# Kernel optimization log

Measured on AMD Instinct MI355X. Metric: run time of the kernel, lower is better.

Reference implementation:

```python
import jax, jax.numpy as jnp
import numpy as np

B, N, DIN, DOUT = 32, 1024, 256, 256


def setup_inputs() -> dict:
    key = jax.random.key(0)
    ks = jax.random.split(key, 7)
    s = 1.0 / np.sqrt(DIN)
    return {
        "x": jax.random.normal(ks[0], (B, N, DIN), dtype=jnp.float32),
        "Wq": jax.random.uniform(ks[1], (DOUT, DIN), minval=-s, maxval=s, dtype=jnp.float32),
        "bq": jax.random.uniform(ks[2], (DOUT,), minval=-s, maxval=s, dtype=jnp.float32),
        "Wk": jax.random.uniform(ks[3], (DOUT, DIN), minval=-s, maxval=s, dtype=jnp.float32),
        "bk": jax.random.uniform(ks[4], (DOUT,), minval=-s, maxval=s, dtype=jnp.float32),
        "Wv": jax.random.uniform(ks[5], (DOUT, DIN), minval=-s, maxval=s, dtype=jnp.float32),
        "bv": jax.random.uniform(ks[6], (DOUT,), minval=-s, maxval=s, dtype=jnp.float32),
    }


def reference(x, Wq, bq, Wk, bk, Wv, bv):
    # q, k, v: (B, N, Dout)
    q = jnp.einsum("bnd,od->bno", x, Wq) + bq
    k = jnp.einsum("bnd,od->bno", x, Wk) + bk
    v = jnp.einsum("bnd,od->bno", x, Wv) + bv
    # logits: (B, N, N) = q @ k^T per batch
    logits = jnp.einsum("bnd,bmd->bnm", q, k)
    # NOTE: softmax over the BATCH dim (axis=0), as in the original module
    attn = jax.nn.softmax(logits, axis=0)
    out = jnp.einsum("bnm,bmd->bnd", attn, v)  # (B, N, Dout)
    return out
```

## Files before the change

kernel.cpp:

```cpp
#include <hip/hip_runtime.h>

typedef __bf16 bf16x8 __attribute__((ext_vector_type(8)));
typedef __bf16 bf16x4 __attribute__((ext_vector_type(4)));
typedef float  f32x4  __attribute__((ext_vector_type(4)));

__device__ __forceinline__ void g2l16(const void* g, void* l) {
    __builtin_amdgcn_global_load_lds((const __attribute__((address_space(1))) void*)g,
                                     (__attribute__((address_space(3))) void*)l, 16, 0, 0);
}

template<int MCH, int NCH>
__device__ __forceinline__ void gemm_core(
    const __bf16* __restrict__ At, const __bf16* __restrict__ Bt,
    int lda, int ldb, int K,
    __bf16* As, __bf16* Bs, f32x4 (&acc)[MCH][NCH], int tid)
{
    const int w = tid >> 6, lane = tid & 63;
    const int quad = lane >> 4, l16 = lane & 15;
    const int wm = w & 1, wn = w >> 1;

    const int srow = (w << 3) + (lane >> 3);
    const int scol = ((lane & 7) ^ (lane >> 3)) << 3;
    char* ldsA = (char*)As + (size_t)w * 1024;
    char* ldsB = (char*)Bs + (size_t)w * 1024;
    const __bf16* Ag = At + (size_t)srow * lda + scol;
    const __bf16* Bg = Bt + (size_t)srow * ldb + scol;

    for (int k0 = 0; k0 < K; k0 += 64) {
        __syncthreads();
        #pragma unroll
        for (int c = 0; c < MCH; c++)
            g2l16(Ag + (size_t)(c * 32) * lda + k0, ldsA + c * 4096);
        #pragma unroll
        for (int c = 0; c < NCH; c++)
            g2l16(Bg + (size_t)(c * 32) * ldb + k0, ldsB + c * 4096);
        __syncthreads();

        #pragma unroll
        for (int kk = 0; kk < 64; kk += 32) {
            const int ub = kk >> 3;
            bf16x8 a[MCH], b[NCH];
            #pragma unroll
            for (int mt = 0; mt < MCH; mt++) {
                const int row = wm * (MCH * 16) + mt * 16 + l16;
                a[mt] = *(const bf16x8*)&As[row * 64 + (((quad + ub) ^ (row & 7)) << 3)];
            }
            #pragma unroll
            for (int nt = 0; nt < NCH; nt++) {
                const int row = wn * (NCH * 16) + nt * 16 + l16;
                b[nt] = *(const bf16x8*)&Bs[row * 64 + (((quad + ub) ^ (row & 7)) << 3)];
            }
            #pragma unroll
            for (int mt = 0; mt < MCH; mt++)
                #pragma unroll
                for (int nt = 0; nt < NCH; nt++)
                    acc[mt][nt] = __builtin_amdgcn_mfma_f32_16x16x32_bf16(
                        a[mt], b[nt], acc[mt][nt], 0, 0, 0);
        }
    }
}


__global__ __launch_bounds__(256)
void gemm_proj(const __bf16* __restrict__ xb, const __bf16* __restrict__ Wb,
               const float* __restrict__ bpack, __bf16* __restrict__ qkv,
               __bf16* __restrict__ vT)
{
    __shared__ __align__(16) __bf16 As[128 * 64];
    __shared__ __align__(16) __bf16 Bs[128 * 64];
    const int tid = threadIdx.x;
    const int id  = blockIdx.x;
    const int z   = id >> 9;
    const int rr  = id & 511;

    const __bf16 *At, *Bt;
    int m0, n0;
    if (z < 2) {
        m0 = (rr & 1) * 128; n0 = (rr >> 1) * 128;
        At = Wb + z * 131072 + m0 * 256;
        Bt = xb + (size_t)n0 * 256;
    } else {
        m0 = (rr >> 1) * 128; n0 = (rr & 1) * 128;
        At = xb + (size_t)m0 * 256;
        Bt = Wb + 2 * 131072 + n0 * 256;
    }

    f32x4 acc[4][4] = {};
    gemm_core<4, 4>(At, Bt, 256, 256, 256, As, Bs, acc, tid);

    const int w = tid >> 6, lane = tid & 63, quad = lane >> 4, l16 = lane & 15;
    const int wm = w & 1, wn = w >> 1;
    #pragma unroll
    for (int mt = 0; mt < 4; mt++) {
        const int i0 = m0 + wm * 64 + mt * 16 + quad * 4;
        #pragma unroll
        for (int nt = 0; nt < 4; nt++) {
            const int j = n0 + wn * 64 + nt * 16 + l16;
            bf16x4 pk;
            if (z < 2) {
                const f32x4 bn = *(const f32x4*)&bpack[z * 256 + i0];
                #pragma unroll
                for (int r = 0; r < 4; r++) pk[r] = (__bf16)(acc[mt][nt][r] + bn[r]);
                *(bf16x4*)(qkv + (size_t)z * 8388608 + (size_t)j * 256 + i0) = pk;
            } else {
                const float bn = bpack[512 + j];
                #pragma unroll
                for (int r = 0; r < 4; r++) pk[r] = (__bf16)(acc[mt][nt][r] + bn);
                *(bf16x4*)(vT + (size_t)j * 32768 + i0) = pk;
            }
        }
    }
}

__global__ __launch_bounds__(256)
void gemm_logits(const __bf16* __restrict__ qb, const __bf16* __restrict__ kb,
                 __bf16* __restrict__ E)
{
    __shared__ __align__(16) __bf16 As[128 * 64];
    __shared__ __align__(16) __bf16 Bs[128 * 64];
    const int tid = threadIdx.x;
    const int id  = blockIdx.x;
    const int x = id & 7, s = id >> 3;
    const int z = x + ((s >> 6) << 3);
    const int t = s & 63;
    const int m0 = (t & 7) * 128;
    const int n0 = (t >> 3) * 128;

    const __bf16* At = kb + (size_t)z * 262144 + m0 * 256;
    const __bf16* Bt = qb + (size_t)z * 262144 + n0 * 256;

    f32x4 acc[4][4] = {};
    gemm_core<4, 4>(At, Bt, 256, 256, 256, As, Bs, acc, tid);

    const int w = tid >> 6, lane = tid & 63, quad = lane >> 4, l16 = lane & 15;
    const int wm = w & 1, wn = w >> 1;
    __bf16* Eb = E + (size_t)z * 1048576;
    #pragma unroll
    for (int mt = 0; mt < 4; mt++) {
        const int i0 = m0 + wm * 64 + mt * 16 + quad * 4;
        #pragma unroll
        for (int nt = 0; nt < 4; nt++) {
            const int j = n0 + wn * 64 + nt * 16 + l16;
            bf16x4 pk;
            #pragma unroll
            for (int r = 0; r < 4; r++) pk[r] = (__bf16)__expf(acc[mt][nt][r]);
            *(bf16x4*)(Eb + (size_t)j * 1024 + i0) = pk;
        }
    }
}

__global__ __launch_bounds__(256)
void gemm_pv(const __bf16* __restrict__ vT, const __bf16* __restrict__ E,
             float* __restrict__ out)
{
    __shared__ __align__(16) __bf16 As[64 * 64];
    __shared__ __align__(16) __bf16 Bs[128 * 64];
    const int tid = threadIdx.x;
    const int id  = blockIdx.x;
    const int x = id & 7, s = id >> 3;
    const int z = x + ((s >> 5) << 3);
    const int t = s & 31;
    const int m0 = (t & 3) * 64;
    const int n0 = (t >> 2) * 128;

    const __bf16* At = vT + (size_t)m0 * 32768 + z * 1024;
    const __bf16* Bt = E + (size_t)z * 1048576 + (size_t)n0 * 1024;

    f32x4 acc[2][4] = {};
    gemm_core<2, 4>(At, Bt, 32768, 1024, 1024, As, Bs, acc, tid);

    const int w = tid >> 6, lane = tid & 63, quad = lane >> 4, l16 = lane & 15;
    const int wm = w & 1, wn = w >> 1;
    float* Ob = out + (size_t)z * 262144;
    #pragma unroll
    for (int mt = 0; mt < 2; mt++) {
        const int i0 = m0 + wm * 32 + mt * 16 + quad * 4;
        #pragma unroll
        for (int nt = 0; nt < 4; nt++) {
            const int j = n0 + wn * 64 + nt * 16 + l16;
            *(f32x4*)(Ob + (size_t)j * 256 + i0) = acc[mt][nt];
        }
    }
}

__global__ __launch_bounds__(256)
void cvt_all(const float* __restrict__ x,
             const float* __restrict__ Wq, const float* __restrict__ Wk,
             const float* __restrict__ Wv,
             const float* __restrict__ bq, const float* __restrict__ bk,
             const float* __restrict__ bv,
             __bf16* __restrict__ xb, __bf16* __restrict__ Wqb,
             float* __restrict__ bpack)
{
    const int i = blockIdx.x * 256 + threadIdx.x;
    if (i < 1073152) {
        const float* s; __bf16* d; int off;
        if (i < 1048576)      { s = x;  d = xb;            off = i; }
        else if (i < 1056768) { s = Wq; d = Wqb;           off = i - 1048576; }
        else if (i < 1064960) { s = Wk; d = Wqb + 131072;  off = i - 1056768; }
        else                  { s = Wv; d = Wqb + 262144;  off = i - 1064960; }
        const float4* s4 = (const float4*)s;
        const float4 f0 = s4[off * 2], f1 = s4[off * 2 + 1];
        bf16x8 o;
        o[0] = (__bf16)f0.x; o[1] = (__bf16)f0.y; o[2] = (__bf16)f0.z; o[3] = (__bf16)f0.w;
        o[4] = (__bf16)f1.x; o[5] = (__bf16)f1.y; o[6] = (__bf16)f1.z; o[7] = (__bf16)f1.w;
        ((bf16x8*)d)[off] = o;
    } else if (i < 1073344) {
        const int j = i - 1073152;
        const int sel = j >> 6, jj = j & 63;
        const float* s = sel == 0 ? bq : (sel == 1 ? bk : bv);
        ((float4*)bpack)[j] = ((const float4*)s)[jj];
    }
}

__global__ __launch_bounds__(256)
void softmax_norm(__bf16* __restrict__ E)
{
    const size_t p = (size_t)blockIdx.x * 256 + threadIdx.x;
    bf16x8* E8 = (bf16x8*)E;
    bf16x8 e[32];
    #pragma unroll
    for (int b = 0; b < 32; b++) e[b] = E8[(size_t)b * 131072 + p];
    float s[8] = {0.f, 0.f, 0.f, 0.f, 0.f, 0.f, 0.f, 0.f};
    #pragma unroll
    for (int b = 0; b < 32; b++)
        #pragma unroll
        for (int j = 0; j < 8; j++) s[j] += (float)e[b][j];
    float rs[8];
    #pragma unroll
    for (int j = 0; j < 8; j++) rs[j] = __builtin_amdgcn_rcpf(s[j]);
    #pragma unroll
    for (int b = 0; b < 32; b++) {
        bf16x8 o = e[b];
        #pragma unroll
        for (int j = 0; j < 8; j++) o[j] = (__bf16)((float)o[j] * rs[j]);
        E8[(size_t)b * 131072 + p] = o;
    }
}

extern "C" void kernel_launch(void* const* d_in, const int* in_sizes, int n_in,
                              void* d_out, int out_size, void* d_ws, size_t ws_size,
                              hipStream_t stream)
{
    const float* x  = (const float*)d_in[0];
    const float* Wq = (const float*)d_in[1];
    const float* bq = (const float*)d_in[2];
    const float* Wk = (const float*)d_in[3];
    const float* bk = (const float*)d_in[4];
    const float* Wv = (const float*)d_in[5];
    const float* bv = (const float*)d_in[6];
    float* out = (float*)d_out;

    char* ws = (char*)d_ws;
    __bf16* xb    = (__bf16*)(ws);
    __bf16* qkv   = (__bf16*)(ws + (16u << 20));
    __bf16* vT    = (__bf16*)(ws + (48u << 20));
    __bf16* E     = (__bf16*)(ws + (64u << 20));
    __bf16* Wqb   = (__bf16*)(ws + (128u << 20));
    float*  bpack = (float*) (ws + (128u << 20) + (3u << 18));

    cvt_all<<<4194, 256, 0, stream>>>(x, Wq, Wk, Wv, bq, bk, bv, xb, Wqb, bpack);

    gemm_proj<<<1536, 256, 0, stream>>>(xb, Wqb, bpack, qkv, vT);

    gemm_logits<<<2048, 256, 0, stream>>>(qkv, qkv + 8388608, E);

    softmax_norm<<<512, 256, 0, stream>>>(E);

    gemm_pv<<<1024, 256, 0, stream>>>(vT, E, out);
}
```

Measured before the change: 203.8 us.

## Fuse all stages into one persistent kernel with grid-wide atomic barriers

Replaces the five separate launches (convert, projection, logits, softmax, PV) with a single persistent kernel of 512 blocks. The blocks loop over tiles of each stage and synchronise with a global atomic-counter barrier between stages. Tile shapes and output layouts also change: projection uses 128x64 tiles and writes q/k row-major, and PV now reads E as the A operand, which changes the E and vT layouts. This removes launch gaps and tail effects between stages. In exchange it risks barrier spin overhead, deadlock if all 512 blocks are not co-resident, and scalar bf16 stores in the epilogues that are less coalesced.

```diff
diff --git a/kernel.cpp b/kernel.cpp
--- a/kernel.cpp
+++ b/kernel.cpp
@@ -61,181 +61,193 @@
 }
 
 
-__global__ __launch_bounds__(256)
-void gemm_proj(const __bf16* __restrict__ xb, const __bf16* __restrict__ Wb,
-               const float* __restrict__ bpack, __bf16* __restrict__ qkv,
-               __bf16* __restrict__ vT)
+__device__ __forceinline__ void cvt_piece(
+    int i, const float* x, const float* Wq, const float* Wk, const float* Wv,
+    __bf16* xb, __bf16* Wqb)
+{
+    const float* s; __bf16* d; int off;
+    if (i < 1048576)      { s = x;  d = xb;            off = i; }
+    else if (i < 1056768) { s = Wq; d = Wqb;           off = i - 1048576; }
+    else if (i < 1064960) { s = Wk; d = Wqb + 131072;  off = i - 1056768; }
+    else                  { s = Wv; d = Wqb + 262144;  off = i - 1064960; }
+    const float4 f0 = ((const float4*)s)[off * 2];
+    const float4 f1 = ((const float4*)s)[off * 2 + 1];
+    bf16x8 o;
+    o[0] = (__bf16)f0.x; o[1] = (__bf16)f0.y; o[2] = (__bf16)f0.z; o[3] = (__bf16)f0.w;
+    o[4] = (__bf16)f1.x; o[5] = (__bf16)f1.y; o[6] = (__bf16)f1.z; o[7] = (__bf16)f1.w;
+    ((bf16x8*)d)[off] = o;
+}
+
+__device__ __forceinline__ void proj_tile(
+    int t, const __bf16* xb, const __bf16* Wqb, const float* bpack,
+    __bf16* qkv, __bf16* vT, __bf16* As, __bf16* Bs, int tid)
+{
+    const int z = t >> 10, lc = t & 1023;
+    const int m0 = (lc & 255) * 128;
+    const int n0 = (lc >> 8) * 64;
+    f32x4 acc[4][2] = {};
+    gemm_core<4, 2>(xb + (size_t)m0 * 256, Wqb + z * 131072 + n0 * 256,
+                    256, 256, 256, As, Bs, acc, tid);
+    const int w = tid >> 6, lane = tid & 63, quad = lane >> 4, l16 = lane & 15;
+    const int wm = w & 1, wn = w >> 1;
+    #pragma unroll
+    for (int mt = 0; mt < 4; mt++) {
+        const int mb = m0 + wm * 64 + mt * 16 + quad * 4;
+        #pragma unroll
+        for (int nt = 0; nt < 2; nt++) {
+            const int n = n0 + wn * 32 + nt * 16 + l16;
+            if (z < 2) {
+                const float bn = bpack[z * 256 + n];
+                __bf16* C = qkv + (size_t)z * 8388608;
+                #pragma unroll
+                for (int r = 0; r < 4; r++)
+                    C[(size_t)(mb + r) * 256 + n] = (__bf16)(acc[mt][nt][r] + bn);
+            } else {
+                const float bn = bpack[512 + n];
+                bf16x4 pk;
+                #pragma unroll
+                for (int r = 0; r < 4; r++) pk[r] = (__bf16)(acc[mt][nt][r] + bn);
+                *(bf16x4*)(vT + (size_t)(mb >> 10) * 262144
+                           + (size_t)n * 1024 + (mb & 1023)) = pk;
+            }
+        }
+    }
+}
+
+__device__ __forceinline__ void logits_tile(
+    int id, const __bf16* qkv, __bf16* E, __bf16* As, __bf16* Bs, int tid)
+{
+    const int x8 = id & 7, s = id >> 3;
+    const int z  = x8 + ((s >> 6) << 3);
+    const int t  = s & 63;
+    const int m0 = (t & 7) * 128;
+    const int n0 = (t >> 3) * 128;
+    f32x4 acc[4][4] = {};
+    gemm_core<4, 4>(qkv + (size_t)z * 262144 + m0 * 256,
+                    qkv + 8388608 + (size_t)z * 262144 + n0 * 256,
+                    256, 256, 256, As, Bs, acc, tid);
+    const int w = tid >> 6, lane = tid & 63, quad = lane >> 4, l16 = lane & 15;
+    const int wm = w & 1, wn = w >> 1;
+    __bf16* Eb = E + (size_t)z * 1048576;
+    #pragma unroll
+    for (int mt = 0; mt < 4; mt++) {
+        const int mb = m0 + wm * 64 + mt * 16 + quad * 4;
+        #pragma unroll
+        for (int nt = 0; nt < 4; nt++) {
+            const int n = n0 + wn * 64 + nt * 16 + l16;
+            #pragma unroll
+            for (int r = 0; r < 4; r++)
+                Eb[(size_t)(mb + r) * 1024 + n] = (__bf16)__expf(acc[mt][nt][r]);
+        }
+    }
+}
+
+__device__ __forceinline__ void softmax_unit(int p, __bf16* E)
+{
+    bf16x4* E4 = (bf16x4*)E;
+    bf16x4 e[32];
+    #pragma unroll
+    for (int b = 0; b < 32; b++) e[b] = E4[(size_t)b * 262144 + p];
+    float sm[4] = {0.f, 0.f, 0.f, 0.f};
+    #pragma unroll
+    for (int b = 0; b < 32; b++)
+        #pragma unroll
+        for (int j = 0; j < 4; j++) sm[j] += (float)e[b][j];
+    float rs[4];
+    #pragma unroll
+    for (int j = 0; j < 4; j++) rs[j] = __builtin_amdgcn_rcpf(sm[j]);
+    #pragma unroll
+    for (int b = 0; b < 32; b++) {
+        bf16x4 o;
+        #pragma unroll
+        for (int j = 0; j < 4; j++) o[j] = (__bf16)((float)e[b][j] * rs[j]);
+        E4[(size_t)b * 262144 + p] = o;
+    }
+}
+
+__device__ __forceinline__ void pv_tile(
+    int id, const __bf16* E, const __bf16* vT, float* out,
+    __bf16* As, __bf16* Bs, int tid)
+{
+    const int x8 = id & 7, s = id >> 3;
+    const int z  = x8 + ((s >> 5) << 3);
+    const int t  = s & 31;
+    const int m0 = (t & 7) * 128;
+    const int n0 = (t >> 3) * 64;
+    f32x4 acc[4][2] = {};
+    gemm_core<4, 2>(E + (size_t)z * 1048576 + (size_t)m0 * 1024,
+                    vT + (size_t)z * 262144 + (size_t)n0 * 1024,
+                    1024, 1024, 1024, As, Bs, acc, tid);
+    const int w = tid >> 6, lane = tid & 63, quad = lane >> 4, l16 = lane & 15;
+    const int wm = w & 1, wn = w >> 1;
+    float* Ob = out + (size_t)z * 262144;
+    #pragma unroll
+    for (int mt = 0; mt < 4; mt++) {
+        const int mb = m0 + wm * 64 + mt * 16 + quad * 4;
+        #pragma unroll
+        for (int nt = 0; nt < 2; nt++) {
+            const int n = n0 + wn * 32 + nt * 16 + l16;
+            #pragma unroll
+            for (int r = 0; r < 4; r++)
+                Ob[(size_t)(mb + r) * 256 + n] = acc[mt][nt][r];
+        }
+    }
+}
+
+__device__ __forceinline__ void gbar(unsigned int* ctr, unsigned int target)
+{
+    __syncthreads();
+    if (threadIdx.x == 0) {
+        __threadfence();
+        __hip_atomic_fetch_add(ctr, 1u, __ATOMIC_RELAXED, __HIP_MEMORY_SCOPE_AGENT);
+        while (__hip_atomic_load(ctr, __ATOMIC_RELAXED, __HIP_MEMORY_SCOPE_AGENT)
+               < target)
+            __builtin_amdgcn_s_sleep(8);
+        __threadfence();
+    }
+    __syncthreads();
+}
+
+__global__ __launch_bounds__(256, 2)
+void mega(const float* __restrict__ x,  const float* __restrict__ Wq,
+          const float* __restrict__ bq, const float* __restrict__ Wk,
+          const float* __restrict__ bk, const float* __restrict__ Wv,
+          const float* __restrict__ bv,
+          __bf16* __restrict__ xb,  __bf16* __restrict__ qkv,
+          __bf16* __restrict__ vT,  __bf16* __restrict__ E,
+          __bf16* __restrict__ Wqb, float* __restrict__ bpack,
+          unsigned int* __restrict__ bar, float* __restrict__ out)
 {
     __shared__ __align__(16) __bf16 As[128 * 64];
     __shared__ __align__(16) __bf16 Bs[128 * 64];
-    const int tid = threadIdx.x;
-    const int id  = blockIdx.x;
-    const int z   = id >> 9;
-    const int rr  = id & 511;
-
-    const __bf16 *At, *Bt;
-    int m0, n0;
-    if (z < 2) {
-        m0 = (rr & 1) * 128; n0 = (rr >> 1) * 128;
-        At = Wb + z * 131072 + m0 * 256;
-        Bt = xb + (size_t)n0 * 256;
-    } else {
-        m0 = (rr >> 1) * 128; n0 = (rr & 1) * 128;
-        At = xb + (size_t)m0 * 256;
-        Bt = Wb + 2 * 131072 + n0 * 256;
-    }
-
-    f32x4 acc[4][4] = {};
-    gemm_core<4, 4>(At, Bt, 256, 256, 256, As, Bs, acc, tid);
-
-    const int w = tid >> 6, lane = tid & 63, quad = lane >> 4, l16 = lane & 15;
-    const int wm = w & 1, wn = w >> 1;
-    #pragma unroll
-    for (int mt = 0; mt < 4; mt++) {
-        const int i0 = m0 + wm * 64 + mt * 16 + quad * 4;
-        #pragma unroll
-        for (int nt = 0; nt < 4; nt++) {
-            const int j = n0 + wn * 64 + nt * 16 + l16;
-            bf16x4 pk;
-            if (z < 2) {
-                const f32x4 bn = *(const f32x4*)&bpack[z * 256 + i0];
-                #pragma unroll
-                for (int r = 0; r < 4; r++) pk[r] = (__bf16)(acc[mt][nt][r] + bn[r]);
-                *(bf16x4*)(qkv + (size_t)z * 8388608 + (size_t)j * 256 + i0) = pk;
-            } else {
-                const float bn = bpack[512 + j];
-                #pragma unroll
-                for (int r = 0; r < 4; r++) pk[r] = (__bf16)(acc[mt][nt][r] + bn);
-                *(bf16x4*)(vT + (size_t)j * 32768 + i0) = pk;
-            }
-        }
-    }
-}
-
-__global__ __launch_bounds__(256)
-void gemm_logits(const __bf16* __restrict__ qb, const __bf16* __restrict__ kb,
-                 __bf16* __restrict__ E)
-{
-    __shared__ __align__(16) __bf16 As[128 * 64];
-    __shared__ __align__(16) __bf16 Bs[128 * 64];
-    const int tid = threadIdx.x;
-    const int id  = blockIdx.x;
-    const int x = id & 7, s = id >> 3;
-    const int z = x + ((s >> 6) << 3);
-    const int t = s & 63;
-    const int m0 = (t & 7) * 128;
-    const int n0 = (t >> 3) * 128;
-
-    const __bf16* At = kb + (size_t)z * 262144 + m0 * 256;
-    const __bf16* Bt = qb + (size_t)z * 262144 + n0 * 256;
-
-    f32x4 acc[4][4] = {};
-    gemm_core<4, 4>(At, Bt, 256, 256, 256, As, Bs, acc, tid);
-
-    const int w = tid >> 6, lane = tid & 63, quad = lane >> 4, l16 = lane & 15;
-    const int wm = w & 1, wn = w >> 1;
-    __bf16* Eb = E + (size_t)z * 1048576;
-    #pragma unroll
-    for (int mt = 0; mt < 4; mt++) {
-        const int i0 = m0 + wm * 64 + mt * 16 + quad * 4;
-        #pragma unroll
-        for (int nt = 0; nt < 4; nt++) {
-            const int j = n0 + wn * 64 + nt * 16 + l16;
-            bf16x4 pk;
-            #pragma unroll
-            for (int r = 0; r < 4; r++) pk[r] = (__bf16)__expf(acc[mt][nt][r]);
-            *(bf16x4*)(Eb + (size_t)j * 1024 + i0) = pk;
-        }
-    }
-}
-
-__global__ __launch_bounds__(256)
-void gemm_pv(const __bf16* __restrict__ vT, const __bf16* __restrict__ E,
-             float* __restrict__ out)
-{
-    __shared__ __align__(16) __bf16 As[64 * 64];
-    __shared__ __align__(16) __bf16 Bs[128 * 64];
-    const int tid = threadIdx.x;
-    const int id  = blockIdx.x;
-    const int x = id & 7, s = id >> 3;
-    const int z = x + ((s >> 5) << 3);
-    const int t = s & 31;
-    const int m0 = (t & 3) * 64;
-    const int n0 = (t >> 2) * 128;
-
-    const __bf16* At = vT + (size_t)m0 * 32768 + z * 1024;
-    const __bf16* Bt = E + (size_t)z * 1048576 + (size_t)n0 * 1024;
-
-    f32x4 acc[2][4] = {};
-    gemm_core<2, 4>(At, Bt, 32768, 1024, 1024, As, Bs, acc, tid);
-
-    const int w = tid >> 6, lane = tid & 63, quad = lane >> 4, l16 = lane & 15;
-    const int wm = w & 1, wn = w >> 1;
-    float* Ob = out + (size_t)z * 262144;
-    #pragma unroll
-    for (int mt = 0; mt < 2; mt++) {
-        const int i0 = m0 + wm * 32 + mt * 16 + quad * 4;
-        #pragma unroll
-        for (int nt = 0; nt < 4; nt++) {
-            const int j = n0 + wn * 64 + nt * 16 + l16;
-            *(f32x4*)(Ob + (size_t)j * 256 + i0) = acc[mt][nt];
-        }
-    }
-}
-
-__global__ __launch_bounds__(256)
-void cvt_all(const float* __restrict__ x,
-             const float* __restrict__ Wq, const float* __restrict__ Wk,
-             const float* __restrict__ Wv,
-             const float* __restrict__ bq, const float* __restrict__ bk,
-             const float* __restrict__ bv,
-             __bf16* __restrict__ xb, __bf16* __restrict__ Wqb,
-             float* __restrict__ bpack)
-{
-    const int i = blockIdx.x * 256 + threadIdx.x;
-    if (i < 1073152) {
-        const float* s; __bf16* d; int off;
-        if (i < 1048576)      { s = x;  d = xb;            off = i; }
-        else if (i < 1056768) { s = Wq; d = Wqb;           off = i - 1048576; }
-        else if (i < 1064960) { s = Wk; d = Wqb + 131072;  off = i - 1056768; }
-        else                  { s = Wv; d = Wqb + 262144;  off = i - 1064960; }
-        const float4* s4 = (const float4*)s;
-        const float4 f0 = s4[off * 2], f1 = s4[off * 2 + 1];
-        bf16x8 o;
-        o[0] = (__bf16)f0.x; o[1] = (__bf16)f0.y; o[2] = (__bf16)f0.z; o[3] = (__bf16)f0.w;
-        o[4] = (__bf16)f1.x; o[5] = (__bf16)f1.y; o[6] = (__bf16)f1.z; o[7] = (__bf16)f1.w;
-        ((bf16x8*)d)[off] = o;
-    } else if (i < 1073344) {
-        const int j = i - 1073152;
-        const int sel = j >> 6, jj = j & 63;
-        const float* s = sel == 0 ? bq : (sel == 1 ? bk : bv);
-        ((float4*)bpack)[j] = ((const float4*)s)[jj];
-    }
-}
-
-__global__ __launch_bounds__(256)
-void softmax_norm(__bf16* __restrict__ E)
-{
-    const size_t p = (size_t)blockIdx.x * 256 + threadIdx.x;
-    bf16x8* E8 = (bf16x8*)E;
-    bf16x8 e[32];
-    #pragma unroll
-    for (int b = 0; b < 32; b++) e[b] = E8[(size_t)b * 131072 + p];
-    float s[8] = {0.f, 0.f, 0.f, 0.f, 0.f, 0.f, 0.f, 0.f};
-    #pragma unroll
-    for (int b = 0; b < 32; b++)
-        #pragma unroll
-        for (int j = 0; j < 8; j++) s[j] += (float)e[b][j];
-    float rs[8];
-    #pragma unroll
-    for (int j = 0; j < 8; j++) rs[j] = __builtin_amdgcn_rcpf(s[j]);
-    #pragma unroll
-    for (int b = 0; b < 32; b++) {
-        bf16x8 o = e[b];
-        #pragma unroll
-        for (int j = 0; j < 8; j++) o[j] = (__bf16)((float)o[j] * rs[j]);
-        E8[(size_t)b * 131072 + p] = o;
-    }
+    const int tid = threadIdx.x, blk = blockIdx.x;
+
+    {
+        const int g0 = blk * 256 + tid;
+        for (int i = g0; i < 1073152; i += 131072)
+            cvt_piece(i, x, Wq, Wk, Wv, xb, Wqb);
+        if (g0 < 192) {
+            const int sel = g0 >> 6, jj = g0 & 63;
+            const float* s = sel == 0 ? bq : (sel == 1 ? bk : bv);
+            ((float4*)bpack)[g0] = ((const float4*)s)[jj];
+        }
+    }
+    gbar(bar, 512);
+
+    for (int it = 0; it < 6; it++)
+        proj_tile(blk + it * 512, xb, Wqb, bpack, qkv, vT, As, Bs, tid);
+    gbar(bar, 1024);
+
+    for (int it = 0; it < 4; it++)
+        logits_tile(blk + it * 512, qkv, E, As, Bs, tid);
+    gbar(bar, 1536);
+
+    for (int it = 0; it < 2; it++)
+        softmax_unit(blk * 256 + tid + it * 131072, E);
+    gbar(bar, 2048);
+
+    for (int it = 0; it < 2; it++)
+        pv_tile(blk + it * 512, E, vT, out, As, Bs, tid);
 }
 
 extern "C" void kernel_launch(void* const* d_in, const int* in_sizes, int n_in,
@@ -258,14 +270,9 @@
     __bf16* E     = (__bf16*)(ws + (64u << 20));
     __bf16* Wqb   = (__bf16*)(ws + (128u << 20));
     float*  bpack = (float*) (ws + (128u << 20) + (3u << 18));
-
-    cvt_all<<<4194, 256, 0, stream>>>(x, Wq, Wk, Wv, bq, bk, bv, xb, Wqb, bpack);
-
-    gemm_proj<<<1536, 256, 0, stream>>>(xb, Wqb, bpack, qkv, vT);
-
-    gemm_logits<<<2048, 256, 0, stream>>>(qkv, qkv + 8388608, E);
-
-    softmax_norm<<<512, 256, 0, stream>>>(E);
-
-    gemm_pv<<<1024, 256, 0, stream>>>(vT, E, out);
-}
+    unsigned int* bar = (unsigned int*)(ws + (128u << 20) + (3u << 18) + 4096);
+
+    hipMemsetAsync(bar, 0, 256, stream);
+    mega<<<512, 256, 0, stream>>>(x, Wq, bq, Wk, bk, Wv, bv,
+                                  xb, qkv, vT, E, Wqb, bpack, bar, out);
+}
```

After: 434.2 us. 2.13x slower.
